# Kernel tuning notes

Hardware: AMD Instinct MI355X
Metric: run time of the kernel (lower is better)

Reference implementation:

```python
import jax, jax.numpy as jnp
import numpy as np

B, N = 1, 768
C_A, C_S, C_Z = 768, 384, 128
H, C_HID, N_TRANS = 16, 48, 2
INF = 1e9
PNAMES = ['attn_s_ln_g', 'attn_ada_gate_w', 'attn_ada_gate_b', 'attn_ada_skip_w',
          'wq', 'bq', 'wk', 'wv', 'z_ln_g', 'z_ln_b', 'wb', 'wg', 'wo',
          'attn_out_gate_w', 'attn_out_gate_b',
          'tr_s_ln_g', 'tr_ada_gate_w', 'tr_ada_gate_b', 'tr_ada_skip_w',
          'tr_w1', 'tr_w2', 'tr_wo', 'tr_out_gate_w', 'tr_out_gate_b']


def _ln(x, eps=1e-5):
    mu = jnp.mean(x, axis=-1, keepdims=True)
    var = jnp.mean((x - mu) ** 2, axis=-1, keepdims=True)
    return (x - mu) * jax.lax.rsqrt(var + eps)


def _adaln(a, s, s_g, gate_w, gate_b, skip_w):
    # AF3 Algorithm 26 AdaLN: a <- LN(a, no affine); s <- LN(s, scale only)
    a_ln = _ln(a)
    s_ln = _ln(s) * s_g
    return jax.nn.sigmoid(s_ln @ gate_w + gate_b) * a_ln + s_ln @ skip_w


def setup_inputs() -> dict:
    key = jax.random.key(0)
    ks = iter(jax.random.split(key, 40))
    w = lambda *sh: jax.random.normal(next(ks), sh, jnp.float32) * 0.02
    return dict(
        a=jax.random.normal(next(ks), (B, N, C_A), jnp.float32),
        s=jax.random.normal(next(ks), (B, N, C_S), jnp.float32),
        z=jax.random.normal(next(ks), (B, N, N, C_Z), jnp.float32),
        mask=jnp.ones((B, N), jnp.int32),
        attn_s_ln_g=jnp.ones((C_S,), jnp.float32),
        attn_ada_gate_w=w(C_S, C_A),
        attn_ada_gate_b=jnp.zeros((C_A,), jnp.float32),
        attn_ada_skip_w=w(C_S, C_A),
        wq=w(C_A, H * C_HID), bq=jnp.zeros((H * C_HID,), jnp.float32),
        wk=w(C_A, H * C_HID), wv=w(C_A, H * C_HID),
        z_ln_g=jnp.ones((C_Z,), jnp.float32), z_ln_b=jnp.zeros((C_Z,), jnp.float32),
        wb=w(C_Z, H), wg=w(C_A, H * C_HID), wo=w(H * C_HID, C_A),
        attn_out_gate_w=w(C_S, C_A),
        attn_out_gate_b=jnp.full((C_A,), -2.0, jnp.float32),  # AdaLN-Zero bias init -2
        tr_s_ln_g=jnp.ones((C_S,), jnp.float32),
        tr_ada_gate_w=w(C_S, C_A),
        tr_ada_gate_b=jnp.zeros((C_A,), jnp.float32),
        tr_ada_skip_w=w(C_S, C_A),
        tr_w1=w(C_A, N_TRANS * C_A), tr_w2=w(C_A, N_TRANS * C_A),
        tr_wo=w(N_TRANS * C_A, C_A),
        tr_out_gate_w=w(C_S, C_A),
        tr_out_gate_b=jnp.full((C_A,), -2.0, jnp.float32),
    )


def _block(a, s, z, maskf, p):
    # --- AttentionPairBias (AF3 Alg 24), residual ---
    a_ln = _adaln(a, s, p['attn_s_ln_g'], p['attn_ada_gate_w'],
                  p['attn_ada_gate_b'], p['attn_ada_skip_w'])
    q = (a_ln @ p['wq'] + p['bq']).reshape(B, N, H, C_HID)
    k = (a_ln @ p['wk']).reshape(B, N, H, C_HID)
    v = (a_ln @ p['wv']).reshape(B, N, H, C_HID)
    pair_bias = (_ln(z) * p['z_ln_g'] + p['z_ln_b']) @ p['wb']  # [B,N,N,H]
    logits = jnp.einsum('bqhc,bkhc->bhqk', q, k) / np.float32(np.sqrt(C_HID))
    logits = logits + jnp.moveaxis(pair_bias, -1, 1)
    logits = logits + (maskf - 1.0)[:, None, None, :] * INF  # mask over keys
    attn = jax.nn.softmax(logits, axis=-1)
    o = jnp.einsum('bhqk,bkhc->bqhc', attn, v)
    g = jax.nn.sigmoid(a_ln @ p['wg']).reshape(B, N, H, C_HID)
    o = (o * g).reshape(B, N, H * C_HID) @ p['wo']
    o = jax.nn.sigmoid(s @ p['attn_out_gate_w'] + p['attn_out_gate_b']) * o
    a = a + o
    # --- ConditionedTransitionBlock (AF3 Alg 25, SwiGLU), residual ---
    t_ln = _adaln(a, s, p['tr_s_ln_g'], p['tr_ada_gate_w'],
                  p['tr_ada_gate_b'], p['tr_ada_skip_w'])
    hid = jax.nn.silu(t_ln @ p['tr_w1']) * (t_ln @ p['tr_w2'])
    t = jax.nn.sigmoid(s @ p['tr_out_gate_w'] + p['tr_out_gate_b']) * (hid @ p['tr_wo'])
    t = t * maskf[..., None]  # _mask_trans=True
    return a + t


def reference(a, s, z, mask, attn_s_ln_g, attn_ada_gate_w, attn_ada_gate_b,
              attn_ada_skip_w, wq, bq, wk, wv, z_ln_g, z_ln_b, wb, wg, wo,
              attn_out_gate_w, attn_out_gate_b, tr_s_ln_g, tr_ada_gate_w,
              tr_ada_gate_b, tr_ada_skip_w, tr_w1, tr_w2, tr_wo,
              tr_out_gate_w, tr_out_gate_b):
    p = dict(zip(PNAMES, (attn_s_ln_g, attn_ada_gate_w, attn_ada_gate_b,
                          attn_ada_skip_w, wq, bq, wk, wv, z_ln_g, z_ln_b, wb,
                          wg, wo, attn_out_gate_w, attn_out_gate_b, tr_s_ln_g,
                          tr_ada_gate_w, tr_ada_gate_b, tr_ada_skip_w, tr_w1,
                          tr_w2, tr_wo, tr_out_gate_w, tr_out_gate_b)))
    return _block(a, s, z, mask.astype(a.dtype), p)
```

## Files before the change

### kernel.cpp

```cpp
#include <hip/hip_runtime.h>
#include <hip/hip_bf16.h>
#include <stdint.h>


typedef __bf16 bf16x8 __attribute__((ext_vector_type(8)));
typedef float  f32x4  __attribute__((ext_vector_type(4)));

#define DEVI __device__ __forceinline__

DEVI uint16_t f2b(float f){ __hip_bfloat16 h = __float2bfloat16(f); return __builtin_bit_cast(uint16_t, h); }
DEVI float    b2f(uint16_t u){ return __bfloat162float(__builtin_bit_cast(__hip_bfloat16, u)); }
DEVI float    sigm(float x){ return 1.0f/(1.0f + __expf(-x)); }

DEVI f32x4 MFMA(uint4 a, uint4 b, f32x4 c){
  return __builtin_amdgcn_mfma_f32_16x16x32_bf16(
      __builtin_bit_cast(bf16x8, a), __builtin_bit_cast(bf16x8, b), c, 0, 0, 0);
}

DEVI void glds16(const void* g, void* l){
  __builtin_amdgcn_global_load_lds(
      (const __attribute__((address_space(1))) void*)g,
      (__attribute__((address_space(3))) void*)l, 16, 0, 0);
}

constexpr size_t SZ_BT_ADA   = (size_t)1536*384*2;
constexpr size_t OFF_BT_ADA_ATTN = 0;
constexpr size_t OFF_BT_ADA_TR   = OFF_BT_ADA_ATTN + SZ_BT_ADA;
constexpr size_t OFF_BT_OUTGATE  = OFF_BT_ADA_TR   + SZ_BT_ADA;
constexpr size_t OFF_BT_QKVG     = OFF_BT_OUTGATE  + SZ_BT_ADA;
constexpr size_t OFF_BT_WO       = OFF_BT_QKVG + (size_t)3072*768*2;
constexpr size_t OFF_BT_W12      = OFF_BT_WO   + (size_t)768*768*2;
constexpr size_t OFF_BT_TRWO     = OFF_BT_W12  + (size_t)3072*768*2;
constexpr size_t OFF_WBGT        = OFF_BT_TRWO + (size_t)768*1536*2;
constexpr size_t OFF_ZCOL        = OFF_WBGT + 4096;
constexpr size_t OFF_OGB         = OFF_ZCOL + 256;
constexpr size_t OFF_SBF         = OFF_OGB + 6144;
constexpr size_t OFF_SLNA        = OFF_SBF  + (size_t)768*384*2;
constexpr size_t OFF_SLNT        = OFF_SLNA + (size_t)768*384*2;
constexpr size_t OFF_GATEOUT     = OFF_SLNT + (size_t)768*384*2;
constexpr size_t OFF_GS          = OFF_GATEOUT + (size_t)768*1536*4;
constexpr size_t OFF_ALNBF       = OFF_GS + (size_t)768*1536*4;
constexpr size_t OFF_QKVGB       = OFF_ALNBF + (size_t)768*768*2;
constexpr size_t OFF_QP          = OFF_QKVGB + (size_t)768*3072*2;
constexpr size_t OFF_KP          = OFF_QP + (size_t)16*768*64*2;
constexpr size_t OFF_VT          = OFF_KP + (size_t)16*768*64*2;
constexpr size_t OFF_BIAS        = OFF_VT + (size_t)16*64*768*2;
constexpr size_t OFF_OBF         = OFF_BIAS + (size_t)16*768*768*2;
constexpr size_t OFF_AMID        = OFF_OBF + (size_t)768*768*2;

struct CvtArgs {
  const float* src[14];
  uint16_t*    dst[14];
  int K[14], N[14];
  int prefix[15];
};

__global__ __launch_bounds__(256) void k_cvt(CvtArgs a){
  int bid = blockIdx.x;
  int ti = 0;
  while (ti < 13 && bid >= a.prefix[ti+1]) ti++;
  int local = bid - a.prefix[ti];
  int K = a.K[ti], N = a.N[ti];
  int tN = N >> 5;
  int n0 = (local % tN) << 5, k0 = (local / tN) << 5;
  __shared__ float lds[32][33];
  const float* src = a.src[ti];
  uint16_t* dst = a.dst[ti];
  int t = threadIdx.x;
  int c = t & 31, r0 = t >> 5;
  #pragma unroll
  for (int i = 0; i < 4; i++){
    int kk = r0 + 8*i;
    lds[kk][c] = src[(size_t)(k0+kk)*N + n0 + c];
  }
  __syncthreads();
  #pragma unroll
  for (int i = 0; i < 4; i++){
    int nn = r0 + 8*i;
    dst[(size_t)(n0+nn)*K + k0 + c] = f2b(lds[c][nn]);
  }
}

__global__ __launch_bounds__(128) void k_prep(
    const float* s, const float* g_attn, const float* g_tr,
    const float* attn_ogb, const float* tr_ogb,
    const float* z_g, const float* z_b, const float* wb,
    uint16_t* s_bf, uint16_t* sln_a, uint16_t* sln_t,
    float* ogb, uint16_t* wbgt, float* zcol)
{
  int b = blockIdx.x, t = threadIdx.x;
  if (b < 768){
    const float* row = s + (size_t)b*384;
    float x0 = row[t], x1 = row[t+128], x2 = row[t+256];
    float sm = x0+x1+x2, sq = x0*x0+x1*x1+x2*x2;
    #pragma unroll
    for (int off = 32; off; off >>= 1){ sm += __shfl_xor(sm, off, 64); sq += __shfl_xor(sq, off, 64); }
    __shared__ float rs_[2], rq_[2];
    int w = t >> 6;
    if ((t & 63) == 0){ rs_[w] = sm; rq_[w] = sq; }
    __syncthreads();
    float S = rs_[0]+rs_[1], Q = rq_[0]+rq_[1];
    float mu = S * (1.f/384.f);
    float var = Q * (1.f/384.f) - mu*mu;
    float rstd = rsqrtf(var + 1e-5f);
    float xs[3] = {x0, x1, x2};
    #pragma unroll
    for (int i = 0; i < 3; i++){
      int ci = t + 128*i;
      float ln = (xs[i] - mu) * rstd;
      s_bf [(size_t)b*384 + ci] = f2b(xs[i]);
      sln_a[(size_t)b*384 + ci] = f2b(ln * g_attn[ci]);
      sln_t[(size_t)b*384 + ci] = f2b(ln * g_tr[ci]);
    }
  } else if (b == 768){
    for (int i = t; i < 1536; i += 128)
      ogb[i] = (i < 768) ? attn_ogb[i] : tr_ogb[i-768];
  } else {
    for (int i = t; i < 2048; i += 128){
      int h = i >> 7, c = i & 127;
      wbgt[i] = f2b(z_g[c] * wb[c*16 + h]);
    }
    if (t < 16){
      float cs = 0.f, cn = 0.f;
      for (int c = 0; c < 128; c++){ cs += z_g[c]*wb[c*16+t]; cn += z_b[c]*wb[c*16+t]; }
      zcol[t] = cs; zcol[16+t] = cn;
    }
  }
}

__global__ __launch_bounds__(256) void k_adaln2(
    const float* __restrict__ asrc, const float* __restrict__ gs,
    const float* __restrict__ gb, uint16_t* __restrict__ out)
{
  int b = blockIdx.x, t = threadIdx.x;
  const float* row = asrc + (size_t)b*768;
  float x0 = row[t], x1 = row[t+256], x2 = row[t+512];
  float sm = x0+x1+x2, sq = x0*x0+x1*x1+x2*x2;
  #pragma unroll
  for (int off = 32; off; off >>= 1){ sm += __shfl_xor(sm, off, 64); sq += __shfl_xor(sq, off, 64); }
  __shared__ float rs_[4], rq_[4];
  int w = t >> 6;
  if ((t & 63) == 0){ rs_[w] = sm; rq_[w] = sq; }
  __syncthreads();
  float S = rs_[0]+rs_[1]+rs_[2]+rs_[3], Q = rq_[0]+rq_[1]+rq_[2]+rq_[3];
  float mu = S*(1.f/768.f), var = Q*(1.f/768.f) - mu*mu, rstd = rsqrtf(var + 1e-5f);
  float xs[3] = {x0, x1, x2};
  #pragma unroll
  for (int i = 0; i < 3; i++){
    int c = t + 256*i;
    float g  = gs[(size_t)b*1536 + c];
    float sk = gs[(size_t)b*1536 + 768 + c];
    out[(size_t)b*768 + c] = f2b(sigm(g + gb[c]) * ((xs[i]-mu)*rstd) + sk);
  }
}

__global__ __launch_bounds__(256) void k_gemm(
    const uint16_t* __restrict__ A, const uint16_t* __restrict__ BT,
    int M, int N, int K,
    float* outF, uint16_t* outB, int mode,
    const float* bias, const float* gate, int gateLd, int gateOff,
    const float* resid, const int* mask)
{
  __shared__ uint16_t As[64*64], Bs[64*64];
  int t = threadIdx.x;
  int n0 = blockIdx.x*64, m0 = blockIdx.y*64;
  int w = t >> 6, lane = t & 63, mm = lane & 15, q = lane >> 4;
  int fc0 = 128*w + lane, fc1 = fc0 + 64;
  int r0 = fc0 >> 3, c0 = (fc0 & 7) ^ (r0 & 7);
  int r1 = fc1 >> 3, c1 = (fc1 & 7) ^ (r1 & 7);
  const uint16_t* gA0 = A  + (size_t)(m0 + r0)*K + c0*8;
  const uint16_t* gA1 = A  + (size_t)(m0 + r1)*K + c1*8;
  const uint16_t* gB0 = BT + (size_t)(n0 + r0)*K + c0*8;
  const uint16_t* gB1 = BT + (size_t)(n0 + r1)*K + c1*8;
  uint16_t* lA0 = As + (2*w + 0)*512;
  uint16_t* lA1 = As + (2*w + 1)*512;
  uint16_t* lB0 = Bs + (2*w + 0)*512;
  uint16_t* lB1 = Bs + (2*w + 1)*512;
  f32x4 zz = {0.f,0.f,0.f,0.f};
  f32x4 acc[4] = {zz, zz, zz, zz};
  int sw = mm & 7;
  for (int k0 = 0; k0 < K; k0 += 64){
    __syncthreads();
    glds16(gA0 + k0, lA0);
    glds16(gA1 + k0, lA1);
    glds16(gB0 + k0, lB0);
    glds16(gB1 + k0, lB1);
    __syncthreads();
    #pragma unroll
    for (int kc = 0; kc < 2; kc++){
      uint4 av = *(const uint4*)&As[(16*w + mm)*64 + ((kc*4 + q) ^ sw)*8];
      #pragma unroll
      for (int j = 0; j < 4; j++){
        uint4 bv = *(const uint4*)&Bs[(16*j + mm)*64 + ((kc*4 + q) ^ sw)*8];
        acc[j] = MFMA(av, bv, acc[j]);
      }
    }
  }
  #pragma unroll
  for (int j = 0; j < 4; j++){
    #pragma unroll
    for (int rr = 0; rr < 4; rr++){
      int row = m0 + 16*w + q*4 + rr;
      int col = n0 + 16*j + mm;
      float v = acc[j][rr];
      size_t oi = (size_t)row*N + col;
      if (mode == 0)      outF[oi] = v;
      else if (mode == 1) outB[oi] = f2b(v);
      else if (mode == 2) outF[oi] = sigm(v + bias[col]);
      else if (mode == 5) outF[oi] = resid[oi] + gate[(size_t)row*gateLd + gateOff + col]*v;
      else {
        float mf = (float)mask[row];
        outF[oi] = resid[oi] + mf * gate[(size_t)row*gateLd + gateOff + col] * v;
      }
    }
  }
}

__global__ __launch_bounds__(256) void k_zbias(
    const float* __restrict__ z, const uint16_t* __restrict__ wbgt_g,
    const float* __restrict__ zcol, uint16_t* __restrict__ bias_g)
{
  __shared__ uint16_t zb[64*128];
  __shared__ uint16_t wbt[16*128];
  __shared__ float mu_s[64], rs_s[64];
  __shared__ uint16_t Sout[16*72];
  int t = threadIdx.x;
  size_t P0 = (size_t)blockIdx.y*768 + (size_t)blockIdx.x*64;
  ((uint4*)wbt)[t] = ((const uint4*)wbgt_g)[t];
  int p = t >> 2, qq = t & 3;
  const float4* zp = (const float4*)(z + (P0 + p)*128) + qq*8;
  float s1 = 0.f, s2 = 0.f;
  uint32_t lb[16];
  #pragma unroll
  for (int it = 0; it < 8; it++){
    float4 v = zp[it];
    s1 += v.x + v.y + v.z + v.w;
    s2 += v.x*v.x + v.y*v.y + v.z*v.z + v.w*v.w;
    lb[2*it]   = (uint32_t)f2b(v.x) | ((uint32_t)f2b(v.y) << 16);
    lb[2*it+1] = (uint32_t)f2b(v.z) | ((uint32_t)f2b(v.w) << 16);
  }
  uint4* zb4 = (uint4*)zb;
  #pragma unroll
  for (int kk = 0; kk < 4; kk++)
    zb4[p*16 + qq*4 + kk] = ((uint4*)lb)[kk];
  s1 += __shfl_xor(s1, 1, 64); s1 += __shfl_xor(s1, 2, 64);
  s2 += __shfl_xor(s2, 1, 64); s2 += __shfl_xor(s2, 2, 64);
  if (qq == 0){
    float mu = s1 * (1.f/128.f);
    mu_s[p] = mu;
    rs_s[p] = rsqrtf(s2*(1.f/128.f) - mu*mu + 1e-5f);
  }
  __syncthreads();
  int w = t >> 6, lane = t & 63, hh = lane & 15, q = lane >> 4;
  float cs = zcol[hh], cn = zcol[16 + hh];
  f32x4 acc = {0.f, 0.f, 0.f, 0.f};
  const uint4* wbt4 = (const uint4*)wbt;
  #pragma unroll
  for (int kc = 0; kc < 4; kc++){
    uint4 av = zb4[(16*w + hh)*16 + kc*4 + q];
    uint4 bv = wbt4[hh*16 + kc*4 + q];
    acc = MFMA(av, bv, acc);
  }
  #pragma unroll
  for (int rr = 0; rr < 4; rr++){
    int pl = 16*w + q*4 + rr;
    float val = rs_s[pl]*(acc[rr] - mu_s[pl]*cs) + cn;
    Sout[hh*72 + pl] = f2b(val);
  }
  __syncthreads();
  int h2 = t >> 4, p2 = (t & 15)*4;
  uint2 v2 = *(uint2*)&Sout[h2*72 + p2];
  *(uint2*)(bias_g + (size_t)h2*589824 + P0 + p2) = v2;
}

__global__ __launch_bounds__(256) void k_trans(
    const uint16_t* __restrict__ qkvg, const float* __restrict__ bq,
    uint16_t* qp, uint16_t* kp, uint16_t* vt)
{
  int h = blockIdx.y, n0 = blockIdx.x*64, t = threadIdx.x;
  __shared__ uint16_t vbuf[64*72];
  int c = t & 63, r0 = t >> 6;
  const float scale = 0.14433756729740643f;
  for (int r = r0; r < 64; r += 4){
    size_t base = (size_t)(n0 + r)*3072;
    float qv = 0.f, kv = 0.f, vv = 0.f;
    if (c < 48){
      int cc = h*48 + c;
      qv = (b2f(qkvg[base + cc]) + bq[cc]) * scale;
      kv = b2f(qkvg[base + 768 + cc]);
      vv = b2f(qkvg[base + 1536 + cc]);
    }
    size_t oi = ((size_t)h*768 + n0 + r)*64 + c;
    qp[oi] = f2b(qv);
    kp[oi] = f2b(kv);
    vbuf[c*72 + r] = f2b(vv);
  }
  __syncthreads();
  int cc = t >> 2, rb = (t & 3)*16;
  uint16_t* dst = vt + ((size_t)h*64 + cc)*768 + n0 + rb;
  *(uint4*)dst       = *(uint4*)&vbuf[cc*72 + rb];
  *(uint4*)(dst + 8) = *(uint4*)&vbuf[cc*72 + rb + 8];
}

__global__ __launch_bounds__(256) void k_flash(
    const uint16_t* __restrict__ qp, const uint16_t* __restrict__ kp,
    const uint16_t* __restrict__ vt, const uint16_t* __restrict__ bias_g,
    const uint16_t* __restrict__ qkvg, const int* __restrict__ mask,
    uint16_t* __restrict__ obf)
{
  __shared__ uint16_t Qs[64*72], Ks[64*72], Vs[64*72], Ps[64*72];
  __shared__ float mk[768];
  int t = threadIdx.x;
  int q0 = blockIdx.x*64, h = blockIdx.y;
  int w = t >> 6, lane = t & 63, mm = lane & 15, q = lane >> 4;
  {
    int row = t >> 2, c = t & 3;
    const uint4* src = (const uint4*)(qp + ((size_t)h*768 + q0 + row)*64) + c*2;
    *(uint4*)&Qs[row*72 + c*16]     = src[0];
    *(uint4*)&Qs[row*72 + c*16 + 8] = src[1];
    mk[t] = (float)mask[t]; mk[t+256] = (float)mask[t+256]; mk[t+512] = (float)mask[t+512];
  }
  f32x4 zz = {0.f,0.f,0.f,0.f};
  f32x4 o0 = zz, o1 = zz, o2 = zz;
  f32x4 m_i = {-1e30f,-1e30f,-1e30f,-1e30f};
  f32x4 l_i = zz;
  const uint16_t* bias_h = bias_g + (size_t)h*589824;
  for (int kt = 0; kt < 12; kt++){
    __syncthreads();
    {
      int row = t >> 2, c = t & 3;
      const uint4* ks = (const uint4*)(kp + ((size_t)h*768 + kt*64 + row)*64) + c*2;
      *(uint4*)&Ks[row*72 + c*16]     = ks[0];
      *(uint4*)&Ks[row*72 + c*16 + 8] = ks[1];
      const uint4* vs = (const uint4*)(vt + ((size_t)h*64 + row)*768 + kt*64) + c*2;
      *(uint4*)&Vs[row*72 + c*16]     = vs[0];
      *(uint4*)&Vs[row*72 + c*16 + 8] = vs[1];
    }
    __syncthreads();
    f32x4 s[4] = {zz, zz, zz, zz};
    #pragma unroll
    for (int kc = 0; kc < 2; kc++){
      uint4 av = *(const uint4*)&Qs[(16*w + mm)*72 + kc*32 + q*8];
      #pragma unroll
      for (int j = 0; j < 4; j++){
        uint4 bv = *(const uint4*)&Ks[(16*j + mm)*72 + kc*32 + q*8];
        s[j] = MFMA(av, bv, s[j]);
      }
    }
    int srow = q0 + 16*w + q*4;
    #pragma unroll
    for (int j = 0; j < 4; j++){
      int scol = kt*64 + 16*j + mm;
      float mt = (mk[scol] - 1.f)*1e9f;
      #pragma unroll
      for (int rr = 0; rr < 4; rr++)
        s[j][rr] += b2f(bias_h[(size_t)(srow+rr)*768 + scol]) + mt;
    }
    f32x4 tm = s[0];
    #pragma unroll
    for (int j = 1; j < 4; j++)
      #pragma unroll
      for (int rr = 0; rr < 4; rr++) tm[rr] = fmaxf(tm[rr], s[j][rr]);
    #pragma unroll
    for (int off = 1; off < 16; off <<= 1)
      #pragma unroll
      for (int rr = 0; rr < 4; rr++) tm[rr] = fmaxf(tm[rr], __shfl_xor(tm[rr], off, 64));
    f32x4 mnew, alpha, rsum = zz;
    #pragma unroll
    for (int rr = 0; rr < 4; rr++){
      mnew[rr] = fmaxf(m_i[rr], tm[rr]);
      alpha[rr] = __expf(m_i[rr] - mnew[rr]);
// ... 30 lines not shown
      o0 = MFMA(av, bv0, o0);
      o1 = MFMA(av, bv1, o1);
      o2 = MFMA(av, bv2, o2);
    }
  }
  f32x4 inv;
  #pragma unroll
  for (int rr = 0; rr < 4; rr++) inv[rr] = 1.f / l_i[rr];
  #pragma unroll
  for (int j = 0; j < 3; j++){
    f32x4 ov = (j == 0) ? o0 : (j == 1) ? o1 : o2;
    int col = 16*j + mm;
    #pragma unroll
    for (int rr = 0; rr < 4; rr++){
      int row = q0 + 16*w + q*4 + rr;
      float g = b2f(qkvg[(size_t)row*3072 + 2304 + h*48 + col]);
      obf[(size_t)row*768 + h*48 + col] = f2b(ov[rr]*inv[rr]*sigm(g));
    }
  }
}

__global__ __launch_bounds__(256) void k_silu(const uint16_t* __restrict__ h12, uint16_t* __restrict__ hid){
  int idx4 = blockIdx.x*256 + threadIdx.x;
  int row = idx4 / 384;
  int c4 = (idx4 % 384)*4;
  const uint16_t* p1 = h12 + (size_t)row*3072 + c4;
  const uint16_t* p2 = p1 + 1536;
  uint16_t o[4];
  #pragma unroll
  for (int i = 0; i < 4; i++){
    float x1 = b2f(p1[i]), x2 = b2f(p2[i]);
    o[i] = f2b(x1*sigm(x1)*x2);
  }
  *(uint2*)(hid + (size_t)row*1536 + c4) = *(uint2*)o;
}

extern "C" void kernel_launch(void* const* d_in, const int* in_sizes, int n_in,
                              void* d_out, int out_size, void* d_ws, size_t ws_size,
                              hipStream_t stream)
{
  const float* a            = (const float*)d_in[0];
  const float* s            = (const float*)d_in[1];
  const float* z            = (const float*)d_in[2];
  const int*   mask         = (const int*)  d_in[3];
  const float* attn_s_ln_g  = (const float*)d_in[4];
  const float* attn_gate_w  = (const float*)d_in[5];
  const float* attn_gate_b  = (const float*)d_in[6];
  const float* attn_skip_w  = (const float*)d_in[7];
  const float* wq           = (const float*)d_in[8];
// ... 20 lines not shown
  char* wsb = (char*)d_ws;
  uint16_t* BTa   = (uint16_t*)(wsb + OFF_BT_ADA_ATTN);
  uint16_t* BTt   = (uint16_t*)(wsb + OFF_BT_ADA_TR);
  uint16_t* BTo   = (uint16_t*)(wsb + OFF_BT_OUTGATE);
  uint16_t* BTq   = (uint16_t*)(wsb + OFF_BT_QKVG);
  uint16_t* BTwo  = (uint16_t*)(wsb + OFF_BT_WO);
  uint16_t* BTw12 = (uint16_t*)(wsb + OFF_BT_W12);
  uint16_t* BTtw  = (uint16_t*)(wsb + OFF_BT_TRWO);
  uint16_t* WBGT  = (uint16_t*)(wsb + OFF_WBGT);
  float*    ZCOL  = (float*)   (wsb + OFF_ZCOL);
  float*    OGB   = (float*)   (wsb + OFF_OGB);
  uint16_t* SBF   = (uint16_t*)(wsb + OFF_SBF);
  uint16_t* SLNA  = (uint16_t*)(wsb + OFF_SLNA);
  uint16_t* SLNT  = (uint16_t*)(wsb + OFF_SLNT);
  float*    GATEOUT=(float*)   (wsb + OFF_GATEOUT);
  float*    GS    = (float*)   (wsb + OFF_GS);
  uint16_t* ALNBF = (uint16_t*)(wsb + OFF_ALNBF);
  uint16_t* QKVGB = (uint16_t*)(wsb + OFF_QKVGB);
  uint16_t* QP    = (uint16_t*)(wsb + OFF_QP);
  uint16_t* KP    = (uint16_t*)(wsb + OFF_KP);
  uint16_t* VT    = (uint16_t*)(wsb + OFF_VT);
  uint16_t* BIASB = (uint16_t*)(wsb + OFF_BIAS);
  uint16_t* OBF   = (uint16_t*)(wsb + OFF_OBF);
  float*    AMID  = (float*)   (wsb + OFF_AMID);
  uint16_t* HIDBF = (uint16_t*)(wsb + OFF_BIAS);
  float*    OUTF  = (float*)d_out;

  CvtArgs ca;
  const float* srcs[14] = {attn_gate_w, attn_skip_w, tr_gate_w, tr_skip_w,
                           attn_og_w, tr_og_w, wq, wk, wv, wg, wo, tr_w1, tr_w2, tr_wo};
  uint16_t* dsts[14] = {BTa, BTa + (size_t)768*384, BTt, BTt + (size_t)768*384,
                        BTo, BTo + (size_t)768*384,
                        BTq, BTq + (size_t)768*768, BTq + (size_t)2*768*768, BTq + (size_t)3*768*768,
                        BTwo, BTw12, BTw12 + (size_t)1536*768, BTtw};
  int Ks[14] = {384,384,384,384,384,384, 768,768,768,768,768, 768,768, 1536};
  int Ns[14] = {768,768,768,768,768,768, 768,768,768,768,768, 1536,1536, 768};
  int tiles[14] = {288,288,288,288,288,288, 576,576,576,576,576, 1152,1152, 1152};
  int pre = 0;
  for (int i = 0; i < 14; i++){
    ca.src[i] = srcs[i]; ca.dst[i] = dsts[i]; ca.K[i] = Ks[i]; ca.N[i] = Ns[i];
    ca.prefix[i] = pre; pre += tiles[i];
  }
  ca.prefix[14] = pre;

  k_cvt<<<pre, 256, 0, stream>>>(ca);
  k_prep<<<770, 128, 0, stream>>>(s, attn_s_ln_g, tr_s_ln_g, attn_og_b, tr_og_b,
                                  z_ln_g, z_ln_b, wb, SBF, SLNA, SLNT, OGB, WBGT, ZCOL);

  k_gemm<<<dim3(24,12), 256, 0, stream>>>(SBF, BTo, 768, 1536, 384,
      GATEOUT, nullptr, 2, OGB, nullptr, 0, 0, nullptr, nullptr);
  k_gemm<<<dim3(24,12), 256, 0, stream>>>(SLNA, BTa, 768, 1536, 384,
      GS, nullptr, 0, nullptr, nullptr, 0, 0, nullptr, nullptr);
  k_adaln2<<<768, 256, 0, stream>>>(a, GS, attn_gate_b, ALNBF);
  k_gemm<<<dim3(48,12), 256, 0, stream>>>(ALNBF, BTq, 768, 3072, 768,
      nullptr, QKVGB, 1, nullptr, nullptr, 0, 0, nullptr, nullptr);

  k_zbias<<<dim3(12,768), 256, 0, stream>>>(z, WBGT, ZCOL, BIASB);
  k_trans<<<dim3(12,16), 256, 0, stream>>>(QKVGB, bq, QP, KP, VT);
  k_flash<<<dim3(12,16), 256, 0, stream>>>(QP, KP, VT, BIASB, QKVGB, mask, OBF);
  k_gemm<<<dim3(12,12), 256, 0, stream>>>(OBF, BTwo, 768, 768, 768,
      AMID, nullptr, 5, nullptr, GATEOUT, 1536, 0, a, nullptr);

  k_gemm<<<dim3(24,12), 256, 0, stream>>>(SLNT, BTt, 768, 1536, 384,
      GS, nullptr, 0, nullptr, nullptr, 0, 0, nullptr, nullptr);
  k_adaln2<<<768, 256, 0, stream>>>(AMID, GS, tr_gate_b, ALNBF);
  k_gemm<<<dim3(48,12), 256, 0, stream>>>(ALNBF, BTw12, 768, 3072, 768,
      nullptr, QKVGB, 1, nullptr, nullptr, 0, 0, nullptr, nullptr);
  k_silu<<<1152, 256, 0, stream>>>(QKVGB, HIDBF);
  k_gemm<<<dim3(12,12), 256, 0, stream>>>(HIDBF, BTtw, 768, 768, 1536,
      OUTF, nullptr, 4, nullptr, GATEOUT, 1536, 768, AMID, mask);
}
```

Before: 632.7 us.

## Merge launches into fused mega-kernels, fuse epilogues, and stage bias in LDS

The weight-conversion and prep kernels are merged into one launch. The z-bias computation is split into two halves that run in the same grids as the adaLN/gate GEMMs and the QKVG GEMM, so they overlap. The QKVG GEMM epilogue now writes head-major Q/K/V^T and the gate directly, which removes the transpose kernel. W1/W2 are interleaved so the SwiGLU is applied in the GEMM epilogue, which removes the separate silu kernel and its round trip through memory. The flash kernel now uses head dim 48 instead of padded 64 and stages bias tiles in LDS. The cost is more complex block dispatch and a larger union LDS footprint per block.

```diff
diff --git a/kernel.cpp b/kernel.cpp
--- a/kernel.cpp
+++ b/kernel.cpp
@@ -38,94 +38,276 @@
 constexpr size_t OFF_SLNA        = OFF_SBF  + (size_t)768*384*2;
 constexpr size_t OFF_SLNT        = OFF_SLNA + (size_t)768*384*2;
 constexpr size_t OFF_GATEOUT     = OFF_SLNT + (size_t)768*384*2;
-constexpr size_t OFF_GS          = OFF_GATEOUT + (size_t)768*1536*4;
-constexpr size_t OFF_ALNBF       = OFF_GS + (size_t)768*1536*4;
-constexpr size_t OFF_QKVGB       = OFF_ALNBF + (size_t)768*768*2;
-constexpr size_t OFF_QP          = OFF_QKVGB + (size_t)768*3072*2;
-constexpr size_t OFF_KP          = OFF_QP + (size_t)16*768*64*2;
-constexpr size_t OFF_VT          = OFF_KP + (size_t)16*768*64*2;
-constexpr size_t OFF_BIAS        = OFF_VT + (size_t)16*64*768*2;
-constexpr size_t OFF_OBF         = OFF_BIAS + (size_t)16*768*768*2;
+constexpr size_t OFF_GSA         = OFF_GATEOUT + (size_t)768*1536*4;
+constexpr size_t OFF_GST         = OFF_GSA + (size_t)768*1536*4;
+constexpr size_t OFF_ALNBF       = OFF_GST + (size_t)768*1536*4;
+constexpr size_t OFF_QP          = OFF_ALNBF + (size_t)768*768*2;
+constexpr size_t OFF_KP          = OFF_QP + (size_t)16*768*48*2;
+constexpr size_t OFF_VT          = OFF_KP + (size_t)16*768*48*2;
+constexpr size_t OFF_GB          = OFF_VT + (size_t)16*48*768*2;
+constexpr size_t OFF_BIASB       = OFF_GB + (size_t)768*768*2;
+constexpr size_t OFF_OBF         = OFF_BIASB + (size_t)16*768*768*2;
 constexpr size_t OFF_AMID        = OFF_OBF + (size_t)768*768*2;
-
-struct CvtArgs {
+constexpr size_t OFF_HID         = OFF_BIASB;
+
+struct PreArgs {
   const float* src[14];
   uint16_t*    dst[14];
-  int K[14], N[14];
+  int K[14], N[14], il[14];
   int prefix[15];
+  int n_cvt;
+  const float *s, *g_attn, *g_tr, *aogb, *togb, *zg, *zb, *wb;
+  uint16_t *s_bf, *sln_a, *sln_t;
+  float* ogb; uint16_t* wbgt; float* zcol;
 };
 
-__global__ __launch_bounds__(256) void k_cvt(CvtArgs a){
-  int bid = blockIdx.x;
-  int ti = 0;
-  while (ti < 13 && bid >= a.prefix[ti+1]) ti++;
-  int local = bid - a.prefix[ti];
-  int K = a.K[ti], N = a.N[ti];
-  int tN = N >> 5;
-  int n0 = (local % tN) << 5, k0 = (local / tN) << 5;
+__global__ __launch_bounds__(256) void k_pre(PreArgs a){
   __shared__ float lds[32][33];
-  const float* src = a.src[ti];
-  uint16_t* dst = a.dst[ti];
-  int t = threadIdx.x;
-  int c = t & 31, r0 = t >> 5;
-  #pragma unroll
-  for (int i = 0; i < 4; i++){
-    int kk = r0 + 8*i;
-    lds[kk][c] = src[(size_t)(k0+kk)*N + n0 + c];
-  }
-  __syncthreads();
-  #pragma unroll
-  for (int i = 0; i < 4; i++){
-    int nn = r0 + 8*i;
-    dst[(size_t)(n0+nn)*K + k0 + c] = f2b(lds[c][nn]);
-  }
-}
-
-__global__ __launch_bounds__(128) void k_prep(
-    const float* s, const float* g_attn, const float* g_tr,
-    const float* attn_ogb, const float* tr_ogb,
-    const float* z_g, const float* z_b, const float* wb,
-    uint16_t* s_bf, uint16_t* sln_a, uint16_t* sln_t,
-    float* ogb, uint16_t* wbgt, float* zcol)
-{
-  int b = blockIdx.x, t = threadIdx.x;
-  if (b < 768){
-    const float* row = s + (size_t)b*384;
-    float x0 = row[t], x1 = row[t+128], x2 = row[t+256];
+  __shared__ float rs_[4], rq_[4];
+  int bid = blockIdx.x, t = threadIdx.x;
+  if (bid < a.n_cvt){
+    int ti = 0;
+    while (ti < 13 && bid >= a.prefix[ti+1]) ti++;
+    int local = bid - a.prefix[ti];
+    int K = a.K[ti], N = a.N[ti], il = a.il[ti];
+    int tN = N >> 5;
+    int n0 = (local % tN) << 5, k0 = (local / tN) << 5;
+    const float* src = a.src[ti];
+    uint16_t* dst = a.dst[ti];
+    int c = t & 31, r0 = t >> 5;
+    #pragma unroll
+    for (int i = 0; i < 4; i++){
+      int kk = r0 + 8*i;
+      lds[kk][c] = src[(size_t)(k0+kk)*N + n0 + c];
+    }
+    __syncthreads();
+    int rbase = (il == 0) ? n0 : (((n0 >> 5) << 6) + ((il == 2) ? 32 : 0));
+    #pragma unroll
+    for (int i = 0; i < 4; i++){
+      int nn = r0 + 8*i;
+      dst[(size_t)(rbase+nn)*K + k0 + c] = f2b(lds[c][nn]);
+    }
+    return;
+  }
+  int b = bid - a.n_cvt;
+  if (b < 384){
+    int row_id = b*2 + (t >> 7);
+    int tt = t & 127;
+    const float* row = a.s + (size_t)row_id*384;
+    float x0 = row[tt], x1 = row[tt+128], x2 = row[tt+256];
     float sm = x0+x1+x2, sq = x0*x0+x1*x1+x2*x2;
     #pragma unroll
     for (int off = 32; off; off >>= 1){ sm += __shfl_xor(sm, off, 64); sq += __shfl_xor(sq, off, 64); }
-    __shared__ float rs_[2], rq_[2];
     int w = t >> 6;
     if ((t & 63) == 0){ rs_[w] = sm; rq_[w] = sq; }
     __syncthreads();
-    float S = rs_[0]+rs_[1], Q = rq_[0]+rq_[1];
+    int base = (t >> 7)*2;
+    float S = rs_[base]+rs_[base+1], Q = rq_[base]+rq_[base+1];
     float mu = S * (1.f/384.f);
     float var = Q * (1.f/384.f) - mu*mu;
     float rstd = rsqrtf(var + 1e-5f);
     float xs[3] = {x0, x1, x2};
     #pragma unroll
     for (int i = 0; i < 3; i++){
-      int ci = t + 128*i;
+      int ci = tt + 128*i;
       float ln = (xs[i] - mu) * rstd;
-      s_bf [(size_t)b*384 + ci] = f2b(xs[i]);
-      sln_a[(size_t)b*384 + ci] = f2b(ln * g_attn[ci]);
-      sln_t[(size_t)b*384 + ci] = f2b(ln * g_tr[ci]);
-    }
-  } else if (b == 768){
-    for (int i = t; i < 1536; i += 128)
-      ogb[i] = (i < 768) ? attn_ogb[i] : tr_ogb[i-768];
+      a.s_bf [(size_t)row_id*384 + ci] = f2b(xs[i]);
+      a.sln_a[(size_t)row_id*384 + ci] = f2b(ln * a.g_attn[ci]);
+      a.sln_t[(size_t)row_id*384 + ci] = f2b(ln * a.g_tr[ci]);
+    }
+  } else if (b == 384){
+    for (int i = t; i < 1536; i += 256)
+      a.ogb[i] = (i < 768) ? a.aogb[i] : a.togb[i-768];
   } else {
-    for (int i = t; i < 2048; i += 128){
+    for (int i = t; i < 2048; i += 256){
       int h = i >> 7, c = i & 127;
-      wbgt[i] = f2b(z_g[c] * wb[c*16 + h]);
+      a.wbgt[i] = f2b(a.zg[c] * a.wb[c*16 + h]);
     }
     if (t < 16){
       float cs = 0.f, cn = 0.f;
-      for (int c = 0; c < 128; c++){ cs += z_g[c]*wb[c*16+t]; cn += z_b[c]*wb[c*16+t]; }
-      zcol[t] = cs; zcol[16+t] = cn;
-    }
-  }
+      for (int c = 0; c < 128; c++){ cs += a.zg[c]*a.wb[c*16+t]; cn += a.zb[c]*a.wb[c*16+t]; }
+      a.zcol[t] = cs; a.zcol[16+t] = cn;
+    }
+  }
+}
+
+struct GemmP {
+  const uint16_t *A, *BT;
+  int N, K, gx, mode, gateLd, gateOff;
+  float* outF; uint16_t* outB;
+  const float *bias, *gate, *resid;
+  const int* mask;
+  uint16_t *qp, *kp, *vt, *gb;
+  const float* bq;
+};
+
+DEVI void gemm_body(const GemmP& p, int bx, int by, uint16_t* As, uint16_t* Bs){
+  int t = threadIdx.x;
+  int n0 = bx*64, m0 = by*64;
+  int w = t >> 6, lane = t & 63, mm = lane & 15, q = lane >> 4;
+  int fc0 = 128*w + lane, fc1 = fc0 + 64;
+  int r0 = fc0 >> 3, c0 = (fc0 & 7) ^ (r0 & 7);
+  int r1 = fc1 >> 3, c1 = (fc1 & 7) ^ (r1 & 7);
+  const uint16_t* gA0 = p.A  + (size_t)(m0 + r0)*p.K + c0*8;
+  const uint16_t* gA1 = p.A  + (size_t)(m0 + r1)*p.K + c1*8;
+  const uint16_t* gB0 = p.BT + (size_t)(n0 + r0)*p.K + c0*8;
+  const uint16_t* gB1 = p.BT + (size_t)(n0 + r1)*p.K + c1*8;
+  uint16_t* lA0 = As + (2*w + 0)*512;
+  uint16_t* lA1 = As + (2*w + 1)*512;
+  uint16_t* lB0 = Bs + (2*w + 0)*512;
+  uint16_t* lB1 = Bs + (2*w + 1)*512;
+  f32x4 zz = {0.f,0.f,0.f,0.f};
+  f32x4 acc[4] = {zz, zz, zz, zz};
+  int sw = mm & 7;
+  for (int k0 = 0; k0 < p.K; k0 += 64){
+    __syncthreads();
+    glds16(gA0 + k0, lA0);
+    glds16(gA1 + k0, lA1);
+    glds16(gB0 + k0, lB0);
+    glds16(gB1 + k0, lB1);
+    __syncthreads();
+    #pragma unroll
+    for (int kc = 0; kc < 2; kc++){
+      uint4 av = *(const uint4*)&As[(16*w + mm)*64 + ((kc*4 + q) ^ sw)*8];
+      #pragma unroll
+      for (int j = 0; j < 4; j++){
+        uint4 bv = *(const uint4*)&Bs[(16*j + mm)*64 + ((kc*4 + q) ^ sw)*8];
+        acc[j] = MFMA(av, bv, acc[j]);
+      }
+    }
+  }
+  if (p.mode == 6){
+    #pragma unroll
+    for (int jj = 0; jj < 2; jj++){
+      #pragma unroll
+      for (int rr = 0; rr < 4; rr++){
+        int row = m0 + 16*w + q*4 + rr;
+        int col = (n0 >> 1) + 16*jj + mm;
+        float x1 = acc[jj][rr], x2 = acc[jj+2][rr];
+        p.outB[(size_t)row*(p.N >> 1) + col] = f2b(x1*sigm(x1)*x2);
+      }
+    }
+    return;
+  }
+  const float scale = 0.14433756729740643f;
+  #pragma unroll
+  for (int j = 0; j < 4; j++){
+    #pragma unroll
+    for (int rr = 0; rr < 4; rr++){
+      int row = m0 + 16*w + q*4 + rr;
+      int col = n0 + 16*j + mm;
+      float v = acc[j][rr];
+      size_t oi = (size_t)row*p.N + col;
+      if (p.mode == 0)      p.outF[oi] = v;
+      else if (p.mode == 2) p.outF[oi] = sigm(v + p.bias[col]);
+      else if (p.mode == 5) p.outF[oi] = p.resid[oi] + p.gate[(size_t)row*p.gateLd + p.gateOff + col]*v;
+      else if (p.mode == 4){
+        float mf = (float)p.mask[row];
+        p.outF[oi] = p.resid[oi] + mf * p.gate[(size_t)row*p.gateLd + p.gateOff + col] * v;
+      } else {
+        if (col < 768){
+          int h = col/48, c = col - h*48;
+          p.qp[((size_t)h*768 + row)*48 + c] = f2b((v + p.bq[col])*scale);
+        } else if (col < 1536){
+          int cc = col - 768; int h = cc/48, c = cc - h*48;
+          p.kp[((size_t)h*768 + row)*48 + c] = f2b(v);
+        } else if (col < 2304){
+          int cc = col - 1536; int h = cc/48, c = cc - h*48;
+          p.vt[((size_t)h*48 + c)*768 + row] = f2b(v);
+        } else {
+          p.gb[(size_t)row*768 + (col - 2304)] = f2b(v);
+        }
+      }
+    }
+  }
+}
+
+__global__ __launch_bounds__(256) void k_gemm(GemmP p){
+  __shared__ __align__(16) uint16_t As[64*64], Bs[64*64];
+  gemm_body(p, blockIdx.x, blockIdx.y, As, Bs);
+}
+
+DEVI void zbias_body(const float* __restrict__ z, const uint16_t* __restrict__ wbgt_g,
+                     const float* __restrict__ zcol, uint16_t* __restrict__ bias_g,
+                     int zbid, uint16_t* zb, uint16_t* wbt, float* mu_s, float* rs_s,
+                     uint16_t* Sout)
+{
+  int t = threadIdx.x;
+  int bx = zbid % 12, by = zbid / 12;
+  size_t P0 = (size_t)by*768 + (size_t)bx*64;
+  ((uint4*)wbt)[t] = ((const uint4*)wbgt_g)[t];
+  int p = t >> 2, qq = t & 3;
+  const float4* zp = (const float4*)(z + (P0 + p)*128) + qq*8;
+  float s1 = 0.f, s2 = 0.f;
+  uint32_t lb[16];
+  #pragma unroll
+  for (int it = 0; it < 8; it++){
+    float4 v = zp[it];
+    s1 += v.x + v.y + v.z + v.w;
+    s2 += v.x*v.x + v.y*v.y + v.z*v.z + v.w*v.w;
+    lb[2*it]   = (uint32_t)f2b(v.x) | ((uint32_t)f2b(v.y) << 16);
+    lb[2*it+1] = (uint32_t)f2b(v.z) | ((uint32_t)f2b(v.w) << 16);
+  }
+  uint4* zb4 = (uint4*)zb;
+  #pragma unroll
+  for (int kk = 0; kk < 4; kk++)
+    zb4[p*16 + qq*4 + kk] = ((uint4*)lb)[kk];
+  s1 += __shfl_xor(s1, 1, 64); s1 += __shfl_xor(s1, 2, 64);
+  s2 += __shfl_xor(s2, 1, 64); s2 += __shfl_xor(s2, 2, 64);
+  if (qq == 0){
+    float mu = s1 * (1.f/128.f);
+    mu_s[p] = mu;
+    rs_s[p] = rsqrtf(s2*(1.f/128.f) - mu*mu + 1e-5f);
+  }
+  __syncthreads();
+  int w = t >> 6, lane = t & 63, hh = lane & 15, q = lane >> 4;
+  float cs = zcol[hh], cn = zcol[16 + hh];
+  f32x4 acc = {0.f, 0.f, 0.f, 0.f};
+  const uint4* wbt4 = (const uint4*)wbt;
+  #pragma unroll
+  for (int kc = 0; kc < 4; kc++){
+    uint4 av = zb4[(16*w + hh)*16 + kc*4 + q];
+    uint4 bv = wbt4[hh*16 + kc*4 + q];
+    acc = MFMA(av, bv, acc);
+  }
+  #pragma unroll
+  for (int rr = 0; rr < 4; rr++){
+    int pl = 16*w + q*4 + rr;
+    float val = rs_s[pl]*(acc[rr] - mu_s[pl]*cs) + cn;
+    Sout[hh*72 + pl] = f2b(val);
+  }
+  __syncthreads();
+  int h2 = t >> 4, p2 = (t & 15)*4;
+  uint2 v2 = *(uint2*)&Sout[h2*72 + p2];
+  *(uint2*)(bias_g + (size_t)h2*589824 + P0 + p2) = v2;
+}
+
+struct ZbP { const float* z; const uint16_t* wbgt; const float* zcol; uint16_t* biasb; int off; };
+struct FatArgs {
+  GemmP g[3];
+  int gstart[4];
+  int gn, gtotal;
+  ZbP zb;
+};
+
+union __align__(16) MegaLds {
+  struct { uint16_t As[64*64], Bs[64*64]; } g;
+  struct { uint16_t zb[64*128]; uint16_t wbt[16*128]; float mu[64], rs[64]; uint16_t Sout[16*72]; } z;
+};
+
+__global__ __launch_bounds__(256) void k_mega(FatArgs fa){
+  __shared__ MegaLds L;
+  int bid = blockIdx.x;
+  if (bid >= fa.gtotal){
+    zbias_body(fa.zb.z, fa.zb.wbgt, fa.zb.zcol, fa.zb.biasb, fa.zb.off + (bid - fa.gtotal),
+               L.z.zb, L.z.wbt, L.z.mu, L.z.rs, L.z.Sout);
+    return;
+  }
+  int gi = 0;
+  while (gi + 1 < fa.gn && bid >= fa.gstart[gi+1]) gi++;
+  GemmP p = fa.g[gi];
+  int local = bid - fa.gstart[gi];
+  gemm_body(p, local % p.gx, local / p.gx, L.g.As, L.g.Bs);
 }
 
 __global__ __launch_bounds__(256) void k_adaln2(
@@ -154,187 +336,54 @@
   }
 }
 
-__global__ __launch_bounds__(256) void k_gemm(
-    const uint16_t* __restrict__ A, const uint16_t* __restrict__ BT,
-    int M, int N, int K,
-    float* outF, uint16_t* outB, int mode,
-    const float* bias, const float* gate, int gateLd, int gateOff,
-    const float* resid, const int* mask)
-{
-  __shared__ uint16_t As[64*64], Bs[64*64];
-  int t = threadIdx.x;
-  int n0 = blockIdx.x*64, m0 = blockIdx.y*64;
-  int w = t >> 6, lane = t & 63, mm = lane & 15, q = lane >> 4;
-  int fc0 = 128*w + lane, fc1 = fc0 + 64;
-  int r0 = fc0 >> 3, c0 = (fc0 & 7) ^ (r0 & 7);
-  int r1 = fc1 >> 3, c1 = (fc1 & 7) ^ (r1 & 7);
-  const uint16_t* gA0 = A  + (size_t)(m0 + r0)*K + c0*8;
-  const uint16_t* gA1 = A  + (size_t)(m0 + r1)*K + c1*8;
-  const uint16_t* gB0 = BT + (size_t)(n0 + r0)*K + c0*8;
-  const uint16_t* gB1 = BT + (size_t)(n0 + r1)*K + c1*8;
-  uint16_t* lA0 = As + (2*w + 0)*512;
-  uint16_t* lA1 = As + (2*w + 1)*512;
-  uint16_t* lB0 = Bs + (2*w + 0)*512;
-  uint16_t* lB1 = Bs + (2*w + 1)*512;
-  f32x4 zz = {0.f,0.f,0.f,0.f};
-  f32x4 acc[4] = {zz, zz, zz, zz};
-  int sw = mm & 7;
-  for (int k0 = 0; k0 < K; k0 += 64){
-    __syncthreads();
-    glds16(gA0 + k0, lA0);
-    glds16(gA1 + k0, lA1);
-    glds16(gB0 + k0, lB0);
-    glds16(gB1 + k0, lB1);
-    __syncthreads();
-    #pragma unroll
-    for (int kc = 0; kc < 2; kc++){
-      uint4 av = *(const uint4*)&As[(16*w + mm)*64 + ((kc*4 + q) ^ sw)*8];
-      #pragma unroll
-      for (int j = 0; j < 4; j++){
-        uint4 bv = *(const uint4*)&Bs[(16*j + mm)*64 + ((kc*4 + q) ^ sw)*8];
-        acc[j] = MFMA(av, bv, acc[j]);
-      }
-    }
-  }
-  #pragma unroll
-  for (int j = 0; j < 4; j++){
-    #pragma unroll
-    for (int rr = 0; rr < 4; rr++){
-      int row = m0 + 16*w + q*4 + rr;
-      int col = n0 + 16*j + mm;
-      float v = acc[j][rr];
-      size_t oi = (size_t)row*N + col;
-      if (mode == 0)      outF[oi] = v;
-      else if (mode == 1) outB[oi] = f2b(v);
-      else if (mode == 2) outF[oi] = sigm(v + bias[col]);
-      else if (mode == 5) outF[oi] = resid[oi] + gate[(size_t)row*gateLd + gateOff + col]*v;
-      else {
-        float mf = (float)mask[row];
-        outF[oi] = resid[oi] + mf * gate[(size_t)row*gateLd + gateOff + col] * v;
-      }
-    }
-  }
-}
-
-__global__ __launch_bounds__(256) void k_zbias(
-    const float* __restrict__ z, const uint16_t* __restrict__ wbgt_g,
-    const float* __restrict__ zcol, uint16_t* __restrict__ bias_g)
-{
-  __shared__ uint16_t zb[64*128];
-  __shared__ uint16_t wbt[16*128];
-  __shared__ float mu_s[64], rs_s[64];
-  __shared__ uint16_t Sout[16*72];
-  int t = threadIdx.x;
-  size_t P0 = (size_t)blockIdx.y*768 + (size_t)blockIdx.x*64;
-  ((uint4*)wbt)[t] = ((const uint4*)wbgt_g)[t];
-  int p = t >> 2, qq = t & 3;
-  const float4* zp = (const float4*)(z + (P0 + p)*128) + qq*8;
-  float s1 = 0.f, s2 = 0.f;
-  uint32_t lb[16];
-  #pragma unroll
-  for (int it = 0; it < 8; it++){
-    float4 v = zp[it];
-    s1 += v.x + v.y + v.z + v.w;
-    s2 += v.x*v.x + v.y*v.y + v.z*v.z + v.w*v.w;
-    lb[2*it]   = (uint32_t)f2b(v.x) | ((uint32_t)f2b(v.y) << 16);
-    lb[2*it+1] = (uint32_t)f2b(v.z) | ((uint32_t)f2b(v.w) << 16);
-  }
-  uint4* zb4 = (uint4*)zb;
-  #pragma unroll
-  for (int kk = 0; kk < 4; kk++)
-    zb4[p*16 + qq*4 + kk] = ((uint4*)lb)[kk];
-  s1 += __shfl_xor(s1, 1, 64); s1 += __shfl_xor(s1, 2, 64);
-  s2 += __shfl_xor(s2, 1, 64); s2 += __shfl_xor(s2, 2, 64);
-  if (qq == 0){
-    float mu = s1 * (1.f/128.f);
-    mu_s[p] = mu;
-    rs_s[p] = rsqrtf(s2*(1.f/128.f) - mu*mu + 1e-5f);
-  }
-  __syncthreads();
-  int w = t >> 6, lane = t & 63, hh = lane & 15, q = lane >> 4;
-  float cs = zcol[hh], cn = zcol[16 + hh];
-  f32x4 acc = {0.f, 0.f, 0.f, 0.f};
-  const uint4* wbt4 = (const uint4*)wbt;
-  #pragma unroll
-  for (int kc = 0; kc < 4; kc++){
-    uint4 av = zb4[(16*w + hh)*16 + kc*4 + q];
-    uint4 bv = wbt4[hh*16 + kc*4 + q];
-    acc = MFMA(av, bv, acc);
-  }
-  #pragma unroll
-  for (int rr = 0; rr < 4; rr++){
-    int pl = 16*w + q*4 + rr;
-    float val = rs_s[pl]*(acc[rr] - mu_s[pl]*cs) + cn;
-    Sout[hh*72 + pl] = f2b(val);
-  }
-  __syncthreads();
-  int h2 = t >> 4, p2 = (t & 15)*4;
-  uint2 v2 = *(uint2*)&Sout[h2*72 + p2];
-  *(uint2*)(bias_g + (size_t)h2*589824 + P0 + p2) = v2;
-}
-
-__global__ __launch_bounds__(256) void k_trans(
-    const uint16_t* __restrict__ qkvg, const float* __restrict__ bq,
-    uint16_t* qp, uint16_t* kp, uint16_t* vt)
-{
-  int h = blockIdx.y, n0 = blockIdx.x*64, t = threadIdx.x;
-  __shared__ uint16_t vbuf[64*72];
-  int c = t & 63, r0 = t >> 6;
-  const float scale = 0.14433756729740643f;
-  for (int r = r0; r < 64; r += 4){
-    size_t base = (size_t)(n0 + r)*3072;
-    float qv = 0.f, kv = 0.f, vv = 0.f;
-    if (c < 48){
-      int cc = h*48 + c;
-      qv = (b2f(qkvg[base + cc]) + bq[cc]) * scale;
-      kv = b2f(qkvg[base + 768 + cc]);
-      vv = b2f(qkvg[base + 1536 + cc]);
-    }
-    size_t oi = ((size_t)h*768 + n0 + r)*64 + c;
-    qp[oi] = f2b(qv);
-    kp[oi] = f2b(kv);
-    vbuf[c*72 + r] = f2b(vv);
-  }
-  __syncthreads();
-  int cc = t >> 2, rb = (t & 3)*16;
-  uint16_t* dst = vt + ((size_t)h*64 + cc)*768 + n0 + rb;
-  *(uint4*)dst       = *(uint4*)&vbuf[cc*72 + rb];
-  *(uint4*)(dst + 8) = *(uint4*)&vbuf[cc*72 + rb + 8];
-}
-
 __global__ __launch_bounds__(256) void k_flash(
     const uint16_t* __restrict__ qp, const uint16_t* __restrict__ kp,
     const uint16_t* __restrict__ vt, const uint16_t* __restrict__ bias_g,
-    const uint16_t* __restrict__ qkvg, const int* __restrict__ mask,
+    const uint16_t* __restrict__ gb, const int* __restrict__ mask,
     uint16_t* __restrict__ obf)
 {
-  __shared__ uint16_t Qs[64*72], Ks[64*72], Vs[64*72], Ps[64*72];
+  __shared__ __align__(16) uint16_t Qs[64*72], Ks[64*72], Vs[48*72], Ps[64*72], Bi[64*72];
   __shared__ float mk[768];
   int t = threadIdx.x;
   int q0 = blockIdx.x*64, h = blockIdx.y;
   int w = t >> 6, lane = t & 63, mm = lane & 15, q = lane >> 4;
   {
-    int row = t >> 2, c = t & 3;
-    const uint4* src = (const uint4*)(qp + ((size_t)h*768 + q0 + row)*64) + c*2;
-    *(uint4*)&Qs[row*72 + c*16]     = src[0];
-    *(uint4*)&Qs[row*72 + c*16 + 8] = src[1];
+    const uint16_t* qbase = qp + ((size_t)h*768 + q0)*48;
+    for (int i = t; i < 384; i += 256){
+      int r = i/6, ch = i - r*6;
+      *(uint4*)&Qs[r*72 + ch*8] = *(const uint4*)&qbase[r*48 + ch*8];
+    }
+    if (t < 128){
+      uint4 z4; z4.x = z4.y = z4.z = z4.w = 0u;
+      int r = t >> 1, off = 48 + (t & 1)*8;
+      *(uint4*)&Qs[r*72 + off] = z4;
+      *(uint4*)&Ks[r*72 + off] = z4;
+    }
     mk[t] = (float)mask[t]; mk[t+256] = (float)mask[t+256]; mk[t+512] = (float)mask[t+512];
   }
   f32x4 zz = {0.f,0.f,0.f,0.f};
   f32x4 o0 = zz, o1 = zz, o2 = zz;
   f32x4 m_i = {-1e30f,-1e30f,-1e30f,-1e30f};
   f32x4 l_i = zz;
-  const uint16_t* bias_h = bias_g + (size_t)h*589824;
+  const uint16_t* bbase0 = bias_g + (size_t)h*589824 + (size_t)q0*768;
   for (int kt = 0; kt < 12; kt++){
     __syncthreads();
     {
-      int row = t >> 2, c = t & 3;
-      const uint4* ks = (const uint4*)(kp + ((size_t)h*768 + kt*64 + row)*64) + c*2;
-      *(uint4*)&Ks[row*72 + c*16]     = ks[0];
-      *(uint4*)&Ks[row*72 + c*16 + 8] = ks[1];
-      const uint4* vs = (const uint4*)(vt + ((size_t)h*64 + row)*768 + kt*64) + c*2;
-      *(uint4*)&Vs[row*72 + c*16]     = vs[0];
-      *(uint4*)&Vs[row*72 + c*16 + 8] = vs[1];
+      const uint16_t* kbase = kp + ((size_t)h*768 + kt*64)*48;
+      for (int i = t; i < 384; i += 256){
+        int r = i/6, ch = i - r*6;
+        *(uint4*)&Ks[r*72 + ch*8] = *(const uint4*)&kbase[r*48 + ch*8];
+      }
+      const uint16_t* vbase = vt + (size_t)h*48*768 + kt*64;
+      for (int i = t; i < 384; i += 256){
+        int r = i >> 3, ch = i & 7;
+        *(uint4*)&Vs[r*72 + ch*8] = *(const uint4*)&vbase[(size_t)r*768 + ch*8];
+      }
+      const uint16_t* bbase = bbase0 + kt*64;
+      for (int i = t; i < 512; i += 256){
+        int r = i >> 3, ch = i & 7;
+        *(uint4*)&Bi[r*72 + ch*8] = *(const uint4*)&bbase[(size_t)r*768 + ch*8];
+      }
     }
     __syncthreads();
     f32x4 s[4] = {zz, zz, zz, zz};
@@ -347,14 +396,14 @@
         s[j] = MFMA(av, bv, s[j]);
       }
     }
-    int srow = q0 + 16*w + q*4;
+    int rbase = 16*w + q*4;
     #pragma unroll
     for (int j = 0; j < 4; j++){
       int scol = kt*64 + 16*j + mm;
       float mt = (mk[scol] - 1.f)*1e9f;
       #pragma unroll
       for (int rr = 0; rr < 4; rr++)
-        s[j][rr] += b2f(bias_h[(size_t)(srow+rr)*768 + scol]) + mt;
+        s[j][rr] += b2f(Bi[(rbase+rr)*72 + 16*j + mm]) + mt;
     }
     f32x4 tm = s[0];
     #pragma unroll
@@ -415,25 +464,10 @@
     #pragma unroll
     for (int rr = 0; rr < 4; rr++){
       int row = q0 + 16*w + q*4 + rr;
-      float g = b2f(qkvg[(size_t)row*3072 + 2304 + h*48 + col]);
+      float g = b2f(gb[(size_t)row*768 + h*48 + col]);
       obf[(size_t)row*768 + h*48 + col] = f2b(ov[rr]*inv[rr]*sigm(g));
     }
   }
-}
-
-__global__ __launch_bounds__(256) void k_silu(const uint16_t* __restrict__ h12, uint16_t* __restrict__ hid){
-  int idx4 = blockIdx.x*256 + threadIdx.x;
-  int row = idx4 / 384;
-  int c4 = (idx4 % 384)*4;
-  const uint16_t* p1 = h12 + (size_t)row*3072 + c4;
-  const uint16_t* p2 = p1 + 1536;
-  uint16_t o[4];
-  #pragma unroll
-  for (int i = 0; i < 4; i++){
-    float x1 = b2f(p1[i]), x2 = b2f(p2[i]);
-    o[i] = f2b(x1*sigm(x1)*x2);
-  }
-  *(uint2*)(hid + (size_t)row*1536 + c4) = *(uint2*)o;
 }
 
 extern "C" void kernel_launch(void* const* d_in, const int* in_sizes, int n_in,
@@ -484,59 +518,98 @@
   uint16_t* SLNA  = (uint16_t*)(wsb + OFF_SLNA);
   uint16_t* SLNT  = (uint16_t*)(wsb + OFF_SLNT);
   float*    GATEOUT=(float*)   (wsb + OFF_GATEOUT);
-  float*    GS    = (float*)   (wsb + OFF_GS);
+  float*    GSA   = (float*)   (wsb + OFF_GSA);
+  float*    GST   = (float*)   (wsb + OFF_GST);
   uint16_t* ALNBF = (uint16_t*)(wsb + OFF_ALNBF);
-  uint16_t* QKVGB = (uint16_t*)(wsb + OFF_QKVGB);
   uint16_t* QP    = (uint16_t*)(wsb + OFF_QP);
   uint16_t* KP    = (uint16_t*)(wsb + OFF_KP);
   uint16_t* VT    = (uint16_t*)(wsb + OFF_VT);
-  uint16_t* BIASB = (uint16_t*)(wsb + OFF_BIAS);
+  uint16_t* GB    = (uint16_t*)(wsb + OFF_GB);
+  uint16_t* BIASB = (uint16_t*)(wsb + OFF_BIASB);
   uint16_t* OBF   = (uint16_t*)(wsb + OFF_OBF);
   float*    AMID  = (float*)   (wsb + OFF_AMID);
-  uint16_t* HIDBF = (uint16_t*)(wsb + OFF_BIAS);
+  uint16_t* HIDBF = (uint16_t*)(wsb + OFF_HID);
   float*    OUTF  = (float*)d_out;
 
-  CvtArgs ca;
+  PreArgs pa;
   const float* srcs[14] = {attn_gate_w, attn_skip_w, tr_gate_w, tr_skip_w,
                            attn_og_w, tr_og_w, wq, wk, wv, wg, wo, tr_w1, tr_w2, tr_wo};
   uint16_t* dsts[14] = {BTa, BTa + (size_t)768*384, BTt, BTt + (size_t)768*384,
                         BTo, BTo + (size_t)768*384,
                         BTq, BTq + (size_t)768*768, BTq + (size_t)2*768*768, BTq + (size_t)3*768*768,
-                        BTwo, BTw12, BTw12 + (size_t)1536*768, BTtw};
+                        BTwo, BTw12, BTw12, BTtw};
   int Ks[14] = {384,384,384,384,384,384, 768,768,768,768,768, 768,768, 1536};
   int Ns[14] = {768,768,768,768,768,768, 768,768,768,768,768, 1536,1536, 768};
+  int il[14] = {0,0,0,0,0,0, 0,0,0,0,0, 1,2, 0};
   int tiles[14] = {288,288,288,288,288,288, 576,576,576,576,576, 1152,1152, 1152};
   int pre = 0;
   for (int i = 0; i < 14; i++){
-    ca.src[i] = srcs[i]; ca.dst[i] = dsts[i]; ca.K[i] = Ks[i]; ca.N[i] = Ns[i];
-    ca.prefix[i] = pre; pre += tiles[i];
-  }
-  ca.prefix[14] = pre;
-
-  k_cvt<<<pre, 256, 0, stream>>>(ca);
-  k_prep<<<770, 128, 0, stream>>>(s, attn_s_ln_g, tr_s_ln_g, attn_og_b, tr_og_b,
-                                  z_ln_g, z_ln_b, wb, SBF, SLNA, SLNT, OGB, WBGT, ZCOL);
-
-  k_gemm<<<dim3(24,12), 256, 0, stream>>>(SBF, BTo, 768, 1536, 384,
-      GATEOUT, nullptr, 2, OGB, nullptr, 0, 0, nullptr, nullptr);
-  k_gemm<<<dim3(24,12), 256, 0, stream>>>(SLNA, BTa, 768, 1536, 384,
-      GS, nullptr, 0, nullptr, nullptr, 0, 0, nullptr, nullptr);
-  k_adaln2<<<768, 256, 0, stream>>>(a, GS, attn_gate_b, ALNBF);
-  k_gemm<<<dim3(48,12), 256, 0, stream>>>(ALNBF, BTq, 768, 3072, 768,
-      nullptr, QKVGB, 1, nullptr, nullptr, 0, 0, nullptr, nullptr);
-
-  k_zbias<<<dim3(12,768), 256, 0, stream>>>(z, WBGT, ZCOL, BIASB);
-  k_trans<<<dim3(12,16), 256, 0, stream>>>(QKVGB, bq, QP, KP, VT);
-  k_flash<<<dim3(12,16), 256, 0, stream>>>(QP, KP, VT, BIASB, QKVGB, mask, OBF);
-  k_gemm<<<dim3(12,12), 256, 0, stream>>>(OBF, BTwo, 768, 768, 768,
-      AMID, nullptr, 5, nullptr, GATEOUT, 1536, 0, a, nullptr);
-
-  k_gemm<<<dim3(24,12), 256, 0, stream>>>(SLNT, BTt, 768, 1536, 384,
-      GS, nullptr, 0, nullptr, nullptr, 0, 0, nullptr, nullptr);
-  k_adaln2<<<768, 256, 0, stream>>>(AMID, GS, tr_gate_b, ALNBF);
-  k_gemm<<<dim3(48,12), 256, 0, stream>>>(ALNBF, BTw12, 768, 3072, 768,
-      nullptr, QKVGB, 1, nullptr, nullptr, 0, 0, nullptr, nullptr);
-  k_silu<<<1152, 256, 0, stream>>>(QKVGB, HIDBF);
-  k_gemm<<<dim3(12,12), 256, 0, stream>>>(HIDBF, BTtw, 768, 768, 1536,
-      OUTF, nullptr, 4, nullptr, GATEOUT, 1536, 768, AMID, mask);
-}
+    pa.src[i] = srcs[i]; pa.dst[i] = dsts[i]; pa.K[i] = Ks[i]; pa.N[i] = Ns[i]; pa.il[i] = il[i];
+    pa.prefix[i] = pre; pre += tiles[i];
+  }
+  pa.prefix[14] = pre;
+  pa.n_cvt = pre;
+  pa.s = s; pa.g_attn = attn_s_ln_g; pa.g_tr = tr_s_ln_g;
+  pa.aogb = attn_og_b; pa.togb = tr_og_b;
+  pa.zg = z_ln_g; pa.zb = z_ln_b; pa.wb = wb;
+  pa.s_bf = SBF; pa.sln_a = SLNA; pa.sln_t = SLNT;
+  pa.ogb = OGB; pa.wbgt = WBGT; pa.zcol = ZCOL;
+  k_pre<<<pre + 386, 256, 0, stream>>>(pa);
+
+  FatArgs f2{};
+  {
+    GemmP p{};
+    p.A = SBF; p.BT = BTo; p.N = 1536; p.K = 384; p.gx = 24; p.mode = 2;
+    p.outF = GATEOUT; p.bias = OGB;
+    f2.g[0] = p;
+    p = GemmP{};
+    p.A = SLNA; p.BT = BTa; p.N = 1536; p.K = 384; p.gx = 24; p.mode = 0; p.outF = GSA;
+    f2.g[1] = p;
+    p = GemmP{};
+    p.A = SLNT; p.BT = BTt; p.N = 1536; p.K = 384; p.gx = 24; p.mode = 0; p.outF = GST;
+    f2.g[2] = p;
+    f2.gstart[0] = 0; f2.gstart[1] = 288; f2.gstart[2] = 576; f2.gstart[3] = 864;
+    f2.gn = 3; f2.gtotal = 864;
+    f2.zb = ZbP{z, WBGT, ZCOL, BIASB, 0};
+  }
+  k_mega<<<864 + 4608, 256, 0, stream>>>(f2);
+
+  k_adaln2<<<768, 256, 0, stream>>>(a, GSA, attn_gate_b, ALNBF);
+
+  FatArgs f4{};
+  {
+    GemmP p{};
+    p.A = ALNBF; p.BT = BTq; p.N = 3072; p.K = 768; p.gx = 48; p.mode = 7;
+    p.qp = QP; p.kp = KP; p.vt = VT; p.gb = GB; p.bq = bq;
+    f4.g[0] = p;
+    f4.gstart[0] = 0; f4.gstart[1] = 576; f4.gn = 1; f4.gtotal = 576;
+    f4.zb = ZbP{z, WBGT, ZCOL, BIASB, 4608};
+  }
+  k_mega<<<576 + 4608, 256, 0, stream>>>(f4);
+
+  k_flash<<<dim3(12,16), 256, 0, stream>>>(QP, KP, VT, BIASB, GB, mask, OBF);
+
+  {
+    GemmP p{};
+    p.A = OBF; p.BT = BTwo; p.N = 768; p.K = 768; p.gx = 12; p.mode = 5;
+    p.outF = AMID; p.gate = GATEOUT; p.gateLd = 1536; p.gateOff = 0; p.resid = a;
+    k_gemm<<<dim3(12,12), 256, 0, stream>>>(p);
+  }
+
+  k_adaln2<<<768, 256, 0, stream>>>(AMID, GST, tr_gate_b, ALNBF);
+
+  {
+    GemmP p{};
+    p.A = ALNBF; p.BT = BTw12; p.N = 3072; p.K = 768; p.gx = 48; p.mode = 6;
+    p.outB = HIDBF;
+    k_gemm<<<dim3(48,12), 256, 0, stream>>>(p);
+  }
+
+  {
+    GemmP p{};
+    p.A = HIDBF; p.BT = BTtw; p.N = 768; p.K = 1536; p.gx = 12; p.mode = 4;
+    p.outF = OUTF; p.gate = GATEOUT; p.gateLd = 1536; p.gateOff = 768;
+    p.resid = AMID; p.mask = mask;
+    k_gemm<<<dim3(12,12), 256, 0, stream>>>(p);
+  }
+}
```

After: 608.3 us. -3.9%, faster.
